# Optimization experiments

Hardware: AMD Instinct MI355X
Metric: run time of the kernel (lower is better)

The kernel has to match this reference:

```python
import jax, jax.numpy as jnp
import numpy as np

N = 100000   # num entities
D = 128      # embed_dim
S = 8192     # num sparse nodes
P = 16       # paths per node (padded; invalid paths fully masked)
K = 16       # max endpoints per path (padded via mask)
H = D // 2   # MLP hidden


def setup_inputs() -> dict:
    key = jax.random.key(0)
    ks = jax.random.split(key, 6)
    entity_embeds = jax.random.normal(ks[0], (N, D), dtype=jnp.float32)
    sparse_ids = jnp.arange(S, dtype=jnp.int32)  # distinct sparse node ids
    endpoint_ids = jax.random.randint(ks[1], (S, P, K), 0, N, dtype=jnp.int32)
    endpoint_mask = jax.random.randint(ks[2], (S, P, K), 0, 2).astype(bool)
    W1 = jax.random.normal(ks[3], (D, H), dtype=jnp.float32) * (1.0 / np.sqrt(D))
    b1 = jnp.zeros((H,), dtype=jnp.float32)
    W2 = jax.random.normal(ks[4], (H, 1), dtype=jnp.float32) * (1.0 / np.sqrt(H))
    b2 = jnp.zeros((1,), dtype=jnp.float32)
    return {"entity_embeds": entity_embeds, "W1": W1, "b1": b1, "W2": W2,
            "b2": b2, "sparse_ids": sparse_ids, "endpoint_ids": endpoint_ids,
            "endpoint_mask": endpoint_mask}


def reference(entity_embeds, W1, b1, W2, b2, sparse_ids, endpoint_ids, endpoint_mask):
    # Gather endpoint embeddings reached by each (sparse node, path): [S,P,K,D]
    gathered = entity_embeds[endpoint_ids]
    m = endpoint_mask.astype(entity_embeds.dtype)[..., None]
    cnt = endpoint_mask.sum(-1)                                   # [S,P] endpoints per path
    agg = (gathered * m).sum(2) / jnp.maximum(cnt, 1)[..., None]  # masked mean [S,P,D]
    # path_weight_net: Linear -> ReLU -> Linear -> Sigmoid (scalar weight per path)
    h = jax.nn.relu(agg @ W1 + b1)                                # [S,P,H]
    w = jax.nn.sigmoid(h @ W2 + b2)                               # [S,P,1]
    valid = cnt > 0                                               # path had endpoints
    feat = jnp.where(valid[..., None], w * agg, 0.0)              # [S,P,D]
    nv = valid.sum(1)                                             # valid paths per node [S]
    node_feat = feat.sum(1) / jnp.maximum(nv, 1)[:, None]         # mean over valid paths
    node_feat = jnp.where((nv > 0)[:, None], node_feat, 0.0)
    # scatter per-sparse-node aggregate into [N,D] (others stay zero)
    remote = jnp.zeros_like(entity_embeds).at[sparse_ids].set(node_feat)
    return remote
```

## Files before the change

kernel.cpp:

```cpp
#include <hip/hip_runtime.h>
#include <hip/hip_bf16.h>

#define S_NODES 8192
#define P_PATHS 16
#define K_EP    16
#define D_DIM   128
#define H_DIM   64

typedef __bf16 bf16x8_t __attribute__((ext_vector_type(8)));
typedef float  f32x4_t  __attribute__((ext_vector_type(4)));

#define AGGF_STRIDE  132
#define AGGBF_STRIDE 136

__global__ __launch_bounds__(256)
void prep_fused_kernel(const float* __restrict__ ent, const float* __restrict__ W1,
                       __bf16* __restrict__ entbf, __bf16* __restrict__ w1t,
                       float4* __restrict__ out4, int n4, int o4)
{
    const int i = blockIdx.x * 256 + threadIdx.x;
    if (i < n4) {
        float4 v = ((const float4*)ent)[i];
        union { __bf16 h[4]; uint2 u; } pk;
        pk.h[0] = (__bf16)v.x; pk.h[1] = (__bf16)v.y;
        pk.h[2] = (__bf16)v.z; pk.h[3] = (__bf16)v.w;
        ((uint2*)entbf)[i] = pk.u;
    }
    if (i < o4) out4[i] = make_float4(0.f, 0.f, 0.f, 0.f);
    if (i < D_DIM * H_DIM) {
        const int n = i >> 7, d = i & 127;
        w1t[i] = (__bf16)W1[d * H_DIM + n];
    }
}

__global__ __launch_bounds__(256)
void prep_w1_kernel(const float* __restrict__ W1, __bf16* __restrict__ w1t)
{
    const int idx = blockIdx.x * 256 + threadIdx.x;
    const int n = idx >> 7, d = idx & 127;
    w1t[idx] = (__bf16)W1[d * H_DIM + n];
}

__device__ __forceinline__ void acc_row(float4& lo, float4& hi, uint4 r)
{
    lo.x += __uint_as_float(r.x << 16); lo.y += __uint_as_float(r.x & 0xffff0000u);
    lo.z += __uint_as_float(r.y << 16); lo.w += __uint_as_float(r.y & 0xffff0000u);
    hi.x += __uint_as_float(r.z << 16); hi.y += __uint_as_float(r.z & 0xffff0000u);
    hi.z += __uint_as_float(r.w << 16); hi.w += __uint_as_float(r.w & 0xffff0000u);
}

__device__ __forceinline__ void merge_xor(float4& v)
{
    v.x += __shfl_xor(v.x, 16); v.y += __shfl_xor(v.y, 16);
    v.z += __shfl_xor(v.z, 16); v.w += __shfl_xor(v.w, 16);
    v.x += __shfl_xor(v.x, 32); v.y += __shfl_xor(v.y, 32);
    v.z += __shfl_xor(v.z, 32); v.w += __shfl_xor(v.w, 32);
}

template<bool USE_BF16>
__global__ __launch_bounds__(256, 8)
void PathGuidedAggregator_kernel(const float*  __restrict__ ent,
                                 const __bf16* __restrict__ entbf,
                                 const float*  __restrict__ b1,
                                 const float*  __restrict__ W2,
                                 const float*  __restrict__ b2,
                                 const int*    __restrict__ sids,
                                 const int*    __restrict__ eids,
                                 const void*   __restrict__ emask,
                                 const __bf16* __restrict__ w1t,
                                 float*        __restrict__ out)
{
    __shared__ float  aggf [P_PATHS][AGGF_STRIDE];
    __shared__ __bf16 aggbf[P_PATHS][AGGBF_STRIDE];
    __shared__ int    cnts[P_PATHS];
    __shared__ int    comp[4][4][K_EP];

    const int s    = blockIdx.x;
    const int tid  = threadIdx.x;
    const int wave = tid >> 6;
    const int lane = tid & 63;

    const unsigned int* mw = (const unsigned int*)emask;
    unsigned int probe = mw[lane];
    const bool floatMask = (__ballot(probe == 0x3F800000u) != 0ULL);
    const bool byteMask  = !floatMask && (__ballot(probe > 1u) != 0ULL);

    const int base = (s * P_PATHS + wave * 4) * K_EP;
    const int idv  = eids[base + lane];
    int mk;
    if (floatMask)     mk = (((const float*)emask)[base + lane] != 0.0f);
    else if (byteMask) mk = ((const unsigned char*)emask)[base + lane];
    else               mk = ((const int*)emask)[base + lane];
    const unsigned long long bits_all = __ballot(mk != 0);

    const int k16  = lane & 15;
    const int pgrp = lane >> 4;
    const unsigned int bits_p = (unsigned int)((bits_all >> (16 * pgrp)) & 0xFFFFu);

    comp[wave][pgrp][k16] = 0;
    if (mk) comp[wave][pgrp][__popc(bits_p & ((1u << k16) - 1u))] = idv;
    if (lane < 4) cnts[wave * 4 + lane] = __popc((unsigned int)((bits_all >> (16 * lane)) & 0xFFFFu));

    const int c0 = __popc((unsigned int)( bits_all        & 0xFFFFu));
    const int c1 = __popc((unsigned int)((bits_all >> 16) & 0xFFFFu));
    const int c2 = __popc((unsigned int)((bits_all >> 32) & 0xFFFFu));
    const int c3 = __popc((unsigned int)((bits_all >> 48) & 0xFFFFu));

    const int q   = lane >> 4;
    const int c16 = lane & 15;

    if constexpr (USE_BF16) {
        const uint4* __restrict__ entb = (const uint4*)entbf + c16;
        float4 l0 = {0,0,0,0}, h0 = l0, l1 = l0, h1 = l0, l2 = l0, h2 = l0, l3 = l0, h3 = l0;
        #pragma unroll
        for (int u = 0; u < 4; ++u) {
            const int slot = q + 4 * u;
            const bool g0 = slot < c0, g1 = slot < c1, g2 = slot < c2, g3 = slot < c3;
            uint4 r0, r1, r2, r3;
            if (g0) r0 = entb[(size_t)comp[wave][0][slot] * 16];
            if (g1) r1 = entb[(size_t)comp[wave][1][slot] * 16];
            if (g2) r2 = entb[(size_t)comp[wave][2][slot] * 16];
            if (g3) r3 = entb[(size_t)comp[wave][3][slot] * 16];
            if (g0) acc_row(l0, h0, r0);
            if (g1) acc_row(l1, h1, r1);
            if (g2) acc_row(l2, h2, r2);
            if (g3) acc_row(l3, h3, r3);
        }
        merge_xor(l0); merge_xor(h0); merge_xor(l1); merge_xor(h1);
        merge_xor(l2); merge_xor(h2); merge_xor(l3); merge_xor(h3);

        const int   cq   = (q == 0) ? c0 : (q == 1) ? c1 : (q == 2) ? c2 : c3;
        const float invq = 1.0f / (float)(cq > 1 ? cq : 1);
        float4 lo = (q == 0) ? l0 : (q == 1) ? l1 : (q == 2) ? l2 : l3;
        float4 hi = (q == 0) ? h0 : (q == 1) ? h1 : (q == 2) ? h2 : h3;
        lo.x *= invq; lo.y *= invq; lo.z *= invq; lo.w *= invq;
        hi.x *= invq; hi.y *= invq; hi.z *= invq; hi.w *= invq;
        const int pw = wave * 4 + q;
        *(float4*)&aggf[pw][c16 * 8]     = lo;
        *(float4*)&aggf[pw][c16 * 8 + 4] = hi;
        union { __bf16 h[8]; uint4 u4; } pk;
        pk.h[0] = (__bf16)lo.x; pk.h[1] = (__bf16)lo.y; pk.h[2] = (__bf16)lo.z; pk.h[3] = (__bf16)lo.w;
        pk.h[4] = (__bf16)hi.x; pk.h[5] = (__bf16)hi.y; pk.h[6] = (__bf16)hi.z; pk.h[7] = (__bf16)hi.w;
        *(uint4*)&aggbf[pw][c16 * 8] = pk.u4;
    } else {
        const int half = lane >> 5;
        const int col  = lane & 31;
        const float4* __restrict__ entc = (const float4*)ent + col;
        float4 acc0 = {0.f,0.f,0.f,0.f}, acc1 = acc0, acc2 = acc0, acc3 = acc0;
        #pragma unroll
        for (int u = 0; u < 8; ++u) {
            const int slot = 2 * u + half;
            const int id0 = comp[wave][0][slot];
            const int id1 = comp[wave][1][slot];
            const int id2 = comp[wave][2][slot];
            const int id3 = comp[wave][3][slot];
            if (slot < c0) { float4 v = entc[(size_t)id0 << 5]; acc0.x += v.x; acc0.y += v.y; acc0.z += v.z; acc0.w += v.w; }
            if (slot < c1) { float4 v = entc[(size_t)id1 << 5]; acc1.x += v.x; acc1.y += v.y; acc1.z += v.z; acc1.w += v.w; }
            if (slot < c2) { float4 v = entc[(size_t)id2 << 5]; acc2.x += v.x; acc2.y += v.y; acc2.z += v.z; acc2.w += v.w; }
            if (slot < c3) { float4 v = entc[(size_t)id3 << 5]; acc3.x += v.x; acc3.y += v.y; acc3.z += v.z; acc3.w += v.w; }
        }
        #pragma unroll
        for (int i = 0; i < 4; ++i) {
            float4 a = (i == 0) ? acc0 : (i == 1) ? acc1 : (i == 2) ? acc2 : acc3;
            const int cnt = (i == 0) ? c0 : (i == 1) ? c1 : (i == 2) ? c2 : c3;
            a.x += __shfl_xor(a.x, 32); a.y += __shfl_xor(a.y, 32);
            a.z += __shfl_xor(a.z, 32); a.w += __shfl_xor(a.w, 32);
            const float inv = 1.0f / (float)(cnt > 1 ? cnt : 1);
            a.x *= inv; a.y *= inv; a.z *= inv; a.w *= inv;
            if (half == 0) {
                const int p = wave * 4 + i;
                *(float4*)&aggf[p][col * 4] = a;
                union { __bf16 h[4]; uint2 u2; } pk;
                pk.h[0] = (__bf16)a.x; pk.h[1] = (__bf16)a.y;
                pk.h[2] = (__bf16)a.z; pk.h[3] = (__bf16)a.w;
                *(uint2*)&aggbf[p][col * 4] = pk.u2;
            }
        }
    }
    __syncthreads();

    if (wave != 0) return;

    const int m    = lane & 15;
    const int quad = lane >> 4;

    bf16x8_t afr[4];
    #pragma unroll
    for (int st = 0; st < 4; ++st)
        afr[st] = *(const bf16x8_t*)&aggbf[m][st * 32 + quad * 8];

    float xp[4] = {0.f, 0.f, 0.f, 0.f};
    #pragma unroll
    for (int t = 0; t < 4; ++t) {
        const int n = t * 16 + m;
        const float b1v = b1[n];
        f32x4_t acc = {b1v, b1v, b1v, b1v};
        const __bf16* bp = w1t + n * D_DIM + quad * 8;
        #pragma unroll
        for (int st = 0; st < 4; ++st) {
            bf16x8_t bfr = *(const bf16x8_t*)(bp + st * 32);
            acc = __builtin_amdgcn_mfma_f32_16x16x32_bf16(afr[st], bfr, acc, 0, 0, 0);
        }
        const float w2v = W2[n];
        #pragma unroll
        for (int r = 0; r < 4; ++r) {
            float h = acc[r] > 0.f ? acc[r] : 0.f;
            xp[r] += h * w2v;
        }
    }
    #pragma unroll
    for (int off = 1; off < 16; off <<= 1) {
        #pragma unroll
        for (int r = 0; r < 4; ++r) xp[r] += __shfl_xor(xp[r], off);
    }

    int myc[4]; int localv = 0;
    #pragma unroll
    for (int r = 0; r < 4; ++r) { myc[r] = cnts[quad * 4 + r]; localv += (myc[r] > 0); }
    int nv = localv + __shfl_xor(localv, 16);
    nv += __shfl_xor(nv, 32);
    const float invnv = 1.0f / (float)(nv > 1 ? nv : 1);
    const float b2v = b2[0];

    float wv[4];
    #pragma unroll
    for (int r = 0; r < 4; ++r) {
        float x = xp[r] + b2v;
        float w = 1.0f / (1.0f + __expf(-x));
        wv[r] = (myc[r] > 0) ? w * invnv : 0.f;
    }

    float fx = 0.f, fy = 0.f;
    #pragma unroll
    for (int p = 0; p < P_PATHS; ++p) {
        float wp = __shfl(wv[p & 3], (p >> 2) << 4);
        float2 a = *(const float2*)&aggf[p][2 * lane];
        fx += wp * a.x; fy += wp * a.y;
    }
    const int row = sids[s];
    *(float2*)&out[(size_t)row * D_DIM + 2 * lane] = make_float2(fx, fy);
}

extern "C" void kernel_launch(void* const* d_in, const int* in_sizes, int n_in,
                              void* d_out, int out_size, void* d_ws, size_t ws_size,
                              hipStream_t stream)
{
    const float* ent  = (const float*)d_in[0];
    const float* W1   = (const float*)d_in[1];
    const float* b1   = (const float*)d_in[2];
    const float* W2   = (const float*)d_in[3];
    const float* b2   = (const float*)d_in[4];
    const int*   sids = (const int*)d_in[5];
    const int*   eids = (const int*)d_in[6];
    const void*  emsk = (const void*)d_in[7];
    float* out = (float*)d_out;

    const int ND = in_sizes[0];
    __bf16* w1t_ws = (__bf16*)d_ws;
    __bf16* entbf  = (__bf16*)((char*)d_ws + 16384);
    const bool useBf16 = (ws_size >= 16384 + (size_t)ND * 2) && ((ND & 3) == 0) && ((out_size & 3) == 0);

    if (useBf16) {
        const int n4 = ND >> 2, o4 = out_size >> 2;
        const int mx = n4 > o4 ? n4 : o4;
        prep_fused_kernel<<<(mx + 255) / 256, 256, 0, stream>>>(ent, W1, entbf, w1t_ws,
                                                                (float4*)out, n4, o4);
        PathGuidedAggregator_kernel<true><<<S_NODES, 256, 0, stream>>>(
            ent, (const __bf16*)entbf, b1, W2, b2, sids, eids, emsk, (const __bf16*)w1t_ws, out);
    } else {
        hipMemsetAsync(d_out, 0, (size_t)out_size * sizeof(float), stream);
        prep_w1_kernel<<<32, 256, 0, stream>>>(W1, w1t_ws);
        PathGuidedAggregator_kernel<false><<<S_NODES, 256, 0, stream>>>(
            ent, (const __bf16*)entbf, b1, W2, b2, sids, eids, emsk, (const __bf16*)w1t_ws, out);
    }
}
```

Before: 175.1 us.

## Use zero sentinel row for branchless prefetched gather of endpoint embeddings

Adds a zeroed extra row at the end of the bf16 entity copy and fills unused compacted slots with its index. The gather loop can then drop its per-slot validity branches and software-pipeline the loads, issuing the next four rows before accumulating the current ones. It also lowers the launch-bounds occupancy hint from 8 to 5 waves so the extra prefetch registers fit. The cost is that every path now always loads 16 rows, with masked slots reading the sentinel row, where before only valid slots were loaded.

```diff
diff --git a/kernel.cpp b/kernel.cpp
--- a/kernel.cpp
+++ b/kernel.cpp
@@ -26,6 +26,8 @@
         pk.h[2] = (__bf16)v.z; pk.h[3] = (__bf16)v.w;
         ((uint2*)entbf)[i] = pk.u;
     }
+    if (i < 32)
+        ((uint2*)entbf)[n4 + i] = make_uint2(0u, 0u);
     if (i < o4) out4[i] = make_float4(0.f, 0.f, 0.f, 0.f);
     if (i < D_DIM * H_DIM) {
         const int n = i >> 7, d = i & 127;
@@ -58,7 +60,7 @@
 }
 
 template<bool USE_BF16>
-__global__ __launch_bounds__(256, 8)
+__global__ __launch_bounds__(256, 5)
 void PathGuidedAggregator_kernel(const float*  __restrict__ ent,
                                  const __bf16* __restrict__ entbf,
                                  const float*  __restrict__ b1,
@@ -68,7 +70,8 @@
                                  const int*    __restrict__ eids,
                                  const void*   __restrict__ emask,
                                  const __bf16* __restrict__ w1t,
-                                 float*        __restrict__ out)
+                                 float*        __restrict__ out,
+                                 int nent)
 {
     __shared__ float  aggf [P_PATHS][AGGF_STRIDE];
     __shared__ __bf16 aggbf[P_PATHS][AGGBF_STRIDE];
@@ -97,7 +100,7 @@
     const int pgrp = lane >> 4;
     const unsigned int bits_p = (unsigned int)((bits_all >> (16 * pgrp)) & 0xFFFFu);
 
-    comp[wave][pgrp][k16] = 0;
+    comp[wave][pgrp][k16] = USE_BF16 ? nent : 0;
     if (mk) comp[wave][pgrp][__popc(bits_p & ((1u << k16) - 1u))] = idv;
     if (lane < 4) cnts[wave * 4 + lane] = __popc((unsigned int)((bits_all >> (16 * lane)) & 0xFFFFu));
 
@@ -112,19 +115,26 @@
     if constexpr (USE_BF16) {
         const uint4* __restrict__ entb = (const uint4*)entbf + c16;
         float4 l0 = {0,0,0,0}, h0 = l0, l1 = l0, h1 = l0, l2 = l0, h2 = l0, l3 = l0, h3 = l0;
+
+        uint4 r0 = entb[(size_t)comp[wave][0][q] * 16];
+        uint4 r1 = entb[(size_t)comp[wave][1][q] * 16];
+        uint4 r2 = entb[(size_t)comp[wave][2][q] * 16];
+        uint4 r3 = entb[(size_t)comp[wave][3][q] * 16];
         #pragma unroll
         for (int u = 0; u < 4; ++u) {
-            const int slot = q + 4 * u;
-            const bool g0 = slot < c0, g1 = slot < c1, g2 = slot < c2, g3 = slot < c3;
-            uint4 r0, r1, r2, r3;
-            if (g0) r0 = entb[(size_t)comp[wave][0][slot] * 16];
-            if (g1) r1 = entb[(size_t)comp[wave][1][slot] * 16];
-            if (g2) r2 = entb[(size_t)comp[wave][2][slot] * 16];
-            if (g3) r3 = entb[(size_t)comp[wave][3][slot] * 16];
-            if (g0) acc_row(l0, h0, r0);
-            if (g1) acc_row(l1, h1, r1);
-            if (g2) acc_row(l2, h2, r2);
-            if (g3) acc_row(l3, h3, r3);
+            uint4 n0, n1, n2, n3;
+            if (u < 3) {
+                const int slot = q + 4 * (u + 1);
+                n0 = entb[(size_t)comp[wave][0][slot] * 16];
+                n1 = entb[(size_t)comp[wave][1][slot] * 16];
+                n2 = entb[(size_t)comp[wave][2][slot] * 16];
+                n3 = entb[(size_t)comp[wave][3][slot] * 16];
+            }
+            acc_row(l0, h0, r0);
+            acc_row(l1, h1, r1);
+            acc_row(l2, h2, r2);
+            acc_row(l3, h3, r3);
+            if (u < 3) { r0 = n0; r1 = n1; r2 = n2; r3 = n3; }
         }
         merge_xor(l0); merge_xor(h0); merge_xor(l1); merge_xor(h1);
         merge_xor(l2); merge_xor(h2); merge_xor(l3); merge_xor(h3);
@@ -255,10 +265,12 @@
     const void*  emsk = (const void*)d_in[7];
     float* out = (float*)d_out;
 
-    const int ND = in_sizes[0];
+    const int ND   = in_sizes[0];
+    const int nent = ND / D_DIM;
     __bf16* w1t_ws = (__bf16*)d_ws;
     __bf16* entbf  = (__bf16*)((char*)d_ws + 16384);
-    const bool useBf16 = (ws_size >= 16384 + (size_t)ND * 2) && ((ND & 3) == 0) && ((out_size & 3) == 0);
+    const bool useBf16 = (ws_size >= 16384 + ((size_t)ND + D_DIM) * 2)
+                         && ((ND & 3) == 0) && ((out_size & 3) == 0);
 
     if (useBf16) {
         const int n4 = ND >> 2, o4 = out_size >> 2;
@@ -266,11 +278,13 @@
         prep_fused_kernel<<<(mx + 255) / 256, 256, 0, stream>>>(ent, W1, entbf, w1t_ws,
                                                                 (float4*)out, n4, o4);
         PathGuidedAggregator_kernel<true><<<S_NODES, 256, 0, stream>>>(
-            ent, (const __bf16*)entbf, b1, W2, b2, sids, eids, emsk, (const __bf16*)w1t_ws, out);
+            ent, (const __bf16*)entbf, b1, W2, b2, sids, eids, emsk,
+            (const __bf16*)w1t_ws, out, nent);
     } else {
         hipMemsetAsync(d_out, 0, (size_t)out_size * sizeof(float), stream);
         prep_w1_kernel<<<32, 256, 0, stream>>>(W1, w1t_ws);
         PathGuidedAggregator_kernel<false><<<S_NODES, 256, 0, stream>>>(
-            ent, (const __bf16*)entbf, b1, W2, b2, sids, eids, emsk, (const __bf16*)w1t_ws, out);
-    }
-}
+            ent, (const __bf16*)entbf, b1, W2, b2, sids, eids, emsk,
+            (const __bf16*)w1t_ws, out, nent);
+    }
+}
```

Result: faster. 169.0 us (-3.4%).
